# Kernel optimization log

Measured on AMD Instinct MI355X. Metric: run time of the kernel, lower is better.

The kernel has to match this reference:

```python
import jax, jax.numpy as jnp
import numpy as np

NUM_HEADS = 8
DEPTH_K = 256
DEPTH_V = 256


def rel_to_abs(x):
    # x: [B, Nh, L, 2L-1] -> [B, Nh, L, L] via the pad/reshape skew trick
    B, Nh, L, _ = x.shape
    x = jnp.pad(x, ((0, 0), (0, 0), (0, 0), (0, 1)))            # [B,Nh,L,2L]
    flat = x.reshape(B, Nh, L * 2 * L)
    flat = jnp.pad(flat, ((0, 0), (0, 0), (0, L - 1)))
    final = flat.reshape(B, Nh, L + 1, 2 * L - 1)
    return final[:, :, :L, L - 1:]


def relative_logits_1d(q, rel_k, H, W, transpose_mask):
    # q: [B, Nh, H, W, d]; rel_k: [2W-1, d]
    B, Nh = q.shape[0], q.shape[1]
    rel = jnp.einsum('bhxyd,md->bhxym', q, rel_k)               # [B,Nh,H,W,2W-1]
    rel = rel.reshape(B, Nh * H, W, 2 * W - 1)
    rel = rel_to_abs(rel)                                       # [B,Nh*H,W,W]
    rel = rel.reshape(B, Nh, H, W, W)
    rel = jnp.broadcast_to(rel[:, :, :, None, :, :], (B, Nh, H, H, W, W))
    rel = jnp.transpose(rel, transpose_mask)
    return rel.reshape(B, Nh, H * W, H * W)


def split_heads_2d(x):
    B, H, W, c = x.shape
    x = x.reshape(B, H, W, NUM_HEADS, c // NUM_HEADS)
    return jnp.transpose(x, (0, 3, 1, 2, 4))                     # [B,Nh,H,W,d]


def setup_inputs() -> dict:
    key = jax.random.key(0)
    k1, k2, k3 = jax.random.split(key, 3)
    dk_head = DEPTH_K // NUM_HEADS
    H = W = 32
    inputs = jax.random.normal(k1, (8, H, W, 2 * DEPTH_K + DEPTH_V), dtype=jnp.float32)
    key_rel_w = jax.random.normal(k2, (2 * W - 1, dk_head), dtype=jnp.float32) * dk_head ** -0.5
    key_rel_h = jax.random.normal(k3, (2 * H - 1, dk_head), dtype=jnp.float32) * dk_head ** -0.5
    return {"inputs": inputs, "key_rel_w": key_rel_w, "key_rel_h": key_rel_h}


def reference(inputs, key_rel_w, key_rel_h):
    B, H, W, _ = inputs.shape
    q, k, v = jnp.split(inputs, [DEPTH_K, 2 * DEPTH_K], axis=-1)
    q = split_heads_2d(q) * (DEPTH_K / NUM_HEADS) ** -0.5        # [B,Nh,H,W,dk]
    k = split_heads_2d(k)
    v = split_heads_2d(v)

    flat_q = q.reshape(B, NUM_HEADS, H * W, -1)
    flat_k = k.reshape(B, NUM_HEADS, H * W, -1)
    flat_v = v.reshape(B, NUM_HEADS, H * W, -1)

    logits = jnp.einsum('bnqd,bnkd->bnqk', flat_q, flat_k)       # [B,Nh,HW,HW]
    w_rel = relative_logits_1d(q, key_rel_w, H, W, (0, 1, 2, 4, 3, 5))
    h_rel = relative_logits_1d(jnp.transpose(q, (0, 1, 3, 2, 4)), key_rel_h,
                               W, H, (0, 1, 4, 2, 5, 3))
    logits = logits + h_rel + w_rel

    weights = jax.nn.softmax(logits, axis=-1)
    attn = jnp.einsum('bnqk,bnkd->bnqd', weights, flat_v)        # [B,Nh,HW,dv]
    attn = attn.reshape(B, NUM_HEADS, H, W, -1)
    out = jnp.transpose(attn, (0, 2, 3, 1, 4)).reshape(B, H, W, DEPTH_V)
    return out
```

## Files before the change

### kernel.cpp

```cpp
#include <hip/hip_runtime.h>
#include <hip/hip_bf16.h>

typedef short bf16x8 __attribute__((ext_vector_type(8)));
typedef float f32x4  __attribute__((ext_vector_type(4)));

#define DEVINL static __device__ __forceinline__

DEVINL unsigned short f2bf(float x){
  union { float f; unsigned u; } v; v.f = x;
  unsigned r = v.u + 0x7fffu + ((v.u >> 16) & 1u);
  return (unsigned short)(r >> 16);
}
DEVINL float bf2f(unsigned short b){
  union { unsigned u; float f; } v; v.u = ((unsigned)b) << 16; return v.f;
}
DEVINL unsigned pk2(float a, float b){
  __hip_bfloat162 h = __float22bfloat162_rn(float2{a, b});
  union { __hip_bfloat162 h2; unsigned u; } cv; cv.h2 = h; return cv.u;
}
DEVINL float fexp2(float x){
  float r; asm("v_exp_f32 %0, %1" : "=v"(r) : "v"(x)); return r;
}

__global__ __launch_bounds__(512, 4)
void aug_attn_kernel(const float* __restrict__ inp,
                     const float* __restrict__ relw,
                     const float* __restrict__ relh,
                     float* __restrict__ out)
{
  __shared__ __align__(16) unsigned short s_rw[128*66];
  __shared__ __align__(16) unsigned short s_rh[128*34];
  __shared__ __align__(16) unsigned short s_k [2][128*40];
  __shared__ __align__(16) unsigned short s_vt[2][4096];

  const int tid  = threadIdx.x;
  const int wv   = tid >> 6;
  const int lane = tid & 63;
  const int lo16 = lane & 15;
  const int hi4  = lane >> 4;

  const int bid = blockIdx.x;
  const int bn  = bid >> 3;
  const int qc  = bid & 7;
  const int b   = bn >> 3;
  const int n   = bn & 7;
  const int x1l = wv >> 1;
  const int qh  = wv & 1;
  const int x1  = qc*4 + x1l;
  const int y1  = qh*16 + lo16;
  const int qrow = x1l*32 + y1;

  const float qscale = 0.17677669529663687f;
  const float L2E    = 1.44269504088896f;
  const float MFIX   = 8.0f;

  const int krow = tid >> 2;
  const int c8   = (tid & 3) * 8;
  const float* kptr = inp + ((size_t)(b*1024 + krow))*768 + 256 + n*32 + c8;
  const float* vptr = kptr + 256;
  const size_t kstep = (size_t)128*768;

  float4 kA = *(const float4*)kptr;
  float4 kB = *(const float4*)(kptr+4);
  float4 vA = *(const float4*)vptr;
  float4 vB = *(const float4*)(vptr+4);

  const int vst = krow >> 6, vkr = krow & 63;
  int vslot[8];
#pragma unroll
  for (int j=0;j<8;++j){
    const int dv = c8 + j;
    vslot[j] = vst*2048 + dv*64 + (((vkr>>3) ^ (dv&7) ^ ((dv>>3)&3))<<3) + (vkr&7);
  }

  bf16x8 qf;
  {
    const float* qp = inp + ((size_t)((b*32 + x1)*32 + y1))*768 + n*32 + hi4*8;
    float4 a = *(const float4*)qp;
    float4 c = *(const float4*)(qp+4);
    union { unsigned u[4]; bf16x8 v; } cv;
    cv.u[0]=pk2(a.x*qscale, a.y*qscale);
    cv.u[1]=pk2(a.z*qscale, a.w*qscale);
    cv.u[2]=pk2(c.x*qscale, c.y*qscale);
    cv.u[3]=pk2(c.z*qscale, c.w*qscale);
    qf = cv.v;
  }

#pragma unroll
  for (int mt=0; mt<4; ++mt){
    const int m = mt*16 + lo16;
    bf16x8 rf = {0,0,0,0,0,0,0,0};
    if (m < 63){
      const float* rp = relw + m*32 + hi4*8;
      float4 a = *(const float4*)rp;
      float4 c = *(const float4*)(rp+4);
      union { unsigned u[4]; bf16x8 v; } cv;
      cv.u[0]=pk2(a.x,a.y); cv.u[1]=pk2(a.z,a.w);
      cv.u[2]=pk2(c.x,c.y); cv.u[3]=pk2(c.z,c.w);
      rf = cv.v;
    }
    f32x4 acc = {0.f,0.f,0.f,0.f};
    acc = __builtin_amdgcn_mfma_f32_16x16x32_bf16(qf, rf, acc, 0,0,0);
    const int rw0 = x1l*32 + qh*16 + hi4*4;
#pragma unroll
    for (int r=0;r<4;++r)
      s_rw[(rw0+r)*66 + m] = f2bf(acc[r]);
  }

#pragma unroll
  for (int mt=0; mt<4; ++mt){
    const int m = mt*16 + lo16;
    bf16x8 rf = {0,0,0,0,0,0,0,0};
    if (m < 63){
      const float* rp = relh + m*32 + hi4*8;
      float4 a = *(const float4*)rp;
      float4 c = *(const float4*)(rp+4);
      union { unsigned u[4]; bf16x8 v; } cv;
      cv.u[0]=pk2(a.x,a.y); cv.u[1]=pk2(a.z,a.w);
      cv.u[2]=pk2(c.x,c.y); cv.u[3]=pk2(c.z,c.w);
      rf = cv.v;
    }
    const int x2 = m + x1 - 31;
    f32x4 acc = {0.f,0.f,0.f,0.f};
    acc = __builtin_amdgcn_mfma_f32_16x16x32_bf16(qf, rf, acc, 0,0,0);
    if (x2 >= 0 && x2 < 32){
      const int rw0 = x1l*32 + qh*16 + hi4*4;
#pragma unroll
      for (int r=0;r<4;++r)
        s_rh[(rw0+r)*34 + x2] = f2bf(acc[r]);
    }
  }

  float rwl2[2][4];
  {
    const int mb = 31 - y1 + 4*hi4;
#pragma unroll
    for (int p=0;p<2;++p)
#pragma unroll
      for (int r=0;r<4;++r)
        rwl2[p][r] = (bf2f(s_rw[qrow*66 + mb + 16*p + r]) - MFIX)*L2E;
  }

  float l_run = 0.f;
  f32x4 accO[2];
  {
    f32x4 z = {0.f,0.f,0.f,0.f};
    accO[0] = z; accO[1] = z;
  }

  for (int ph=0; ph<8; ++ph){
    const int cur = ph & 1;
    {
      uint4 kw; kw.x=pk2(kA.x,kA.y); kw.y=pk2(kA.z,kA.w);
                kw.z=pk2(kB.x,kB.y); kw.w=pk2(kB.z,kB.w);
      *(uint4*)(&s_k[cur][krow*40 + c8]) = kw;
      const unsigned u0=pk2(vA.x,vA.y), u1=pk2(vA.z,vA.w);
      const unsigned u2=pk2(vB.x,vB.y), u3=pk2(vB.z,vB.w);
      unsigned short* vt = s_vt[cur];
      vt[vslot[0]]=(unsigned short)u0;  vt[vslot[1]]=(unsigned short)(u0>>16);
      vt[vslot[2]]=(unsigned short)u1;  vt[vslot[3]]=(unsigned short)(u1>>16);
      vt[vslot[4]]=(unsigned short)u2;  vt[vslot[5]]=(unsigned short)(u2>>16);
      vt[vslot[6]]=(unsigned short)u3;  vt[vslot[7]]=(unsigned short)(u3>>16);
    }
    asm volatile("s_waitcnt lgkmcnt(0)" ::: "memory");
    __builtin_amdgcn_s_barrier();
    asm volatile("" ::: "memory");

    if (ph < 7){
      kptr += kstep; vptr += kstep;
      kA = *(const float4*)kptr; kB = *(const float4*)(kptr+4);
      vA = *(const float4*)vptr; vB = *(const float4*)(vptr+4);
    }

#pragma unroll
    for (int st=0; st<2; ++st){
      bf16x8 kfrag[4];
#pragma unroll
      for (int kt=0;kt<4;++kt)
        kfrag[kt] = *(const bf16x8*)(&s_k[cur][(st*64 + kt*16 + lo16)*40 + hi4*8]);
      bf16x8 vfrag[2][2];
#pragma unroll
      for (int dvt=0;dvt<2;++dvt){
        const int dv = dvt*16 + lo16;
        const int xr = (dv&7) ^ ((dv>>3)&3);
#pragma unroll
        for (int kc=0;kc<2;++kc){
          const int blk = (kc*4 + hi4) ^ xr;
          vfrag[dvt][kc] = *(const bf16x8*)(&s_vt[cur][st*2048 + dv*64 + blk*8]);
        }
      }

      f32x4 S[4];
      __builtin_amdgcn_s_setprio(1);
#pragma unroll
      for (int kt=0;kt<4;++kt){
        f32x4 z = {0.f,0.f,0.f,0.f};
        S[kt] = __builtin_amdgcn_mfma_f32_16x16x32_bf16(kfrag[kt], qf, z, 0,0,0);
      }
      __builtin_amdgcn_s_setprio(0);

      const unsigned rhu = *(const unsigned*)(&s_rh[qrow*34 + 4*ph + 2*st]);
      const float rh0L = bf2f((unsigned short)(rhu & 0xffffu))*L2E;
      const float rh1L = bf2f((unsigned short)(rhu >> 16))*L2E;
      unsigned W[4][2];
      float lacc = 0.f;
#pragma unroll
      for (int kt=0;kt<4;++kt){
        const float rhL = (kt<2)? rh0L : rh1L;
        const int p = kt & 1;
        float pv0 = fexp2(__builtin_fmaf(S[kt][0], L2E, rwl2[p][0] + rhL));
        float pv1 = fexp2(__builtin_fmaf(S[kt][1], L2E, rwl2[p][1] + rhL));
        float pv2 = fexp2(__builtin_fmaf(S[kt][2], L2E, rwl2[p][2] + rhL));
        float pv3 = fexp2(__builtin_fmaf(S[kt][3], L2E, rwl2[p][3] + rhL));
        lacc += (pv0+pv1) + (pv2+pv3);
        W[kt][0] = pk2(pv0, pv1);
        W[kt][1] = pk2(pv2, pv3);
      }
      l_run += lacc;

      bf16x8 pfrag[2];
#pragma unroll
      for (int kc=0;kc<2;++kc){
        unsigned r0 = W[2*kc][0],   r1 = W[2*kc][1];
        unsigned r2 = W[2*kc+1][0], r3 = W[2*kc+1][1];
        asm("v_permlane32_swap_b32 %0, %1" : "+v"(r0), "+v"(r2));
        asm("v_permlane32_swap_b32 %0, %1" : "+v"(r1), "+v"(r3));
        asm("v_permlane16_swap_b32 %0, %1" : "+v"(r0), "+v"(r2));
        asm("v_permlane16_swap_b32 %0, %1" : "+v"(r1), "+v"(r3));
        union { unsigned u[4]; bf16x8 v; } cv;
        cv.u[0]=r0; cv.u[1]=r1; cv.u[2]=r2; cv.u[3]=r3;
        pfrag[kc] = cv.v;
      }

      __builtin_amdgcn_s_setprio(1);
#pragma unroll
      for (int kc=0;kc<2;++kc)
#pragma unroll
        for (int dvt=0;dvt<2;++dvt)
          accO[dvt] = __builtin_amdgcn_mfma_f32_16x16x32_bf16(
                        vfrag[dvt][kc], pfrag[kc], accO[dvt], 0,0,0);
      __builtin_amdgcn_s_setprio(0);
    }
  }

  float l = l_run;
  l += __shfl_xor(l, 16, 64);
  l += __shfl_xor(l, 32, 64);
  const float inv = 1.f / l;
  float* op = out + ((size_t)((b*32 + x1)*32 + y1))*256 + n*32;
#pragma unroll
  for (int dvt=0;dvt<2;++dvt){
    float4 o;
    o.x = accO[dvt][0]*inv;
    o.y = accO[dvt][1]*inv;
    o.z = accO[dvt][2]*inv;
    o.w = accO[dvt][3]*inv;
    *(float4*)(op + dvt*16 + hi4*4) = o;
  }
}

extern "C" void kernel_launch(void* const* d_in, const int* in_sizes, int n_in,
                              void* d_out, int out_size, void* d_ws, size_t ws_size,
                              hipStream_t stream) {
  (void)in_sizes; (void)n_in; (void)d_ws; (void)ws_size; (void)out_size;
  const float* inp  = (const float*)d_in[0];
  const float* relw = (const float*)d_in[1];
  const float* relh = (const float*)d_in[2];
  float* out = (float*)d_out;
  dim3 grid(512), block(512);
  aug_attn_kernel<<<grid, block, 0, stream>>>(inp, relw, relh, out);
}
```

Baseline: 100.7 us.

## Deepen K/V prefetch to two stages, remap blocks per XCD, drop setprio

Global loads for K/V now run two tiles ahead using two register sets, and the LDS store for the next tile moves to the end of each phase, after the compute. This hides more global-load latency behind the MFMA and exp work. The block index is remapped so that the eight query chunks of one (batch, head) land on the same XCD, which improves L2 reuse of K/V. The s_setprio hints are removed and the phase loop is fully unrolled, at the cost of higher register pressure that could reduce occupancy.

```diff
diff --git a/kernel.cpp b/kernel.cpp
--- a/kernel.cpp
+++ b/kernel.cpp
@@ -39,9 +39,11 @@
   const int lo16 = lane & 15;
   const int hi4  = lane >> 4;
 
-  const int bid = blockIdx.x;
-  const int bn  = bid >> 3;
-  const int qc  = bid & 7;
+  const int p   = blockIdx.x;
+  const int xcd = p & 7;
+  const int j   = p >> 3;
+  const int bn  = xcd*8 + (j >> 3);
+  const int qc  = j & 7;
   const int b   = bn >> 3;
   const int n   = bn & 7;
   const int x1l = wv >> 1;
@@ -56,22 +58,24 @@
 
   const int krow = tid >> 2;
   const int c8   = (tid & 3) * 8;
-  const float* kptr = inp + ((size_t)(b*1024 + krow))*768 + 256 + n*32 + c8;
-  const float* vptr = kptr + 256;
+  const float* kbase = inp + ((size_t)(b*1024 + krow))*768 + 256 + n*32 + c8;
   const size_t kstep = (size_t)128*768;
-
-  float4 kA = *(const float4*)kptr;
-  float4 kB = *(const float4*)(kptr+4);
-  float4 vA = *(const float4*)vptr;
-  float4 vB = *(const float4*)(vptr+4);
 
   const int vst = krow >> 6, vkr = krow & 63;
   int vslot[8];
 #pragma unroll
-  for (int j=0;j<8;++j){
-    const int dv = c8 + j;
-    vslot[j] = vst*2048 + dv*64 + (((vkr>>3) ^ (dv&7) ^ ((dv>>3)&3))<<3) + (vkr&7);
-  }
+  for (int jj=0;jj<8;++jj){
+    const int dv = c8 + jj;
+    vslot[jj] = vst*2048 + dv*64 + (((vkr>>3) ^ (dv&7) ^ ((dv>>3)&3))<<3) + (vkr&7);
+  }
+
+  float4 kR0a, kR0b, vR0a, vR0b;
+  float4 kR1a, kR1b, vR1a, vR1b;
+
+  kR0a = *(const float4*)(kbase);
+  kR0b = *(const float4*)(kbase+4);
+  vR0a = *(const float4*)(kbase+256);
+  vR0b = *(const float4*)(kbase+260);
 
   bf16x8 qf;
   {
@@ -135,10 +139,30 @@
   {
     const int mb = 31 - y1 + 4*hi4;
 #pragma unroll
-    for (int p=0;p<2;++p)
+    for (int pp=0;pp<2;++pp)
 #pragma unroll
       for (int r=0;r<4;++r)
-        rwl2[p][r] = (bf2f(s_rw[qrow*66 + mb + 16*p + r]) - MFIX)*L2E;
+        rwl2[pp][r] = (bf2f(s_rw[qrow*66 + mb + 16*pp + r]) - MFIX)*L2E;
+  }
+
+  {
+    uint4 kw; kw.x=pk2(kR0a.x,kR0a.y); kw.y=pk2(kR0a.z,kR0a.w);
+              kw.z=pk2(kR0b.x,kR0b.y); kw.w=pk2(kR0b.z,kR0b.w);
+    *(uint4*)(&s_k[0][krow*40 + c8]) = kw;
+    const unsigned u0=pk2(vR0a.x,vR0a.y), u1=pk2(vR0a.z,vR0a.w);
+    const unsigned u2=pk2(vR0b.x,vR0b.y), u3=pk2(vR0b.z,vR0b.w);
+    unsigned short* vt = s_vt[0];
+    vt[vslot[0]]=(unsigned short)u0;  vt[vslot[1]]=(unsigned short)(u0>>16);
+    vt[vslot[2]]=(unsigned short)u1;  vt[vslot[3]]=(unsigned short)(u1>>16);
+    vt[vslot[4]]=(unsigned short)u2;  vt[vslot[5]]=(unsigned short)(u2>>16);
+    vt[vslot[6]]=(unsigned short)u3;  vt[vslot[7]]=(unsigned short)(u3>>16);
+  }
+  {
+    const float* kp = kbase + kstep;
+    kR1a = *(const float4*)(kp);
+    kR1b = *(const float4*)(kp+4);
+    vR1a = *(const float4*)(kp+256);
+    vR1b = *(const float4*)(kp+260);
   }
 
   float l_run = 0.f;
@@ -148,28 +172,22 @@
     accO[0] = z; accO[1] = z;
   }
 
+#pragma unroll
   for (int ph=0; ph<8; ++ph){
     const int cur = ph & 1;
-    {
-      uint4 kw; kw.x=pk2(kA.x,kA.y); kw.y=pk2(kA.z,kA.w);
-                kw.z=pk2(kB.x,kB.y); kw.w=pk2(kB.z,kB.w);
-      *(uint4*)(&s_k[cur][krow*40 + c8]) = kw;
-      const unsigned u0=pk2(vA.x,vA.y), u1=pk2(vA.z,vA.w);
-      const unsigned u2=pk2(vB.x,vB.y), u3=pk2(vB.z,vB.w);
-      unsigned short* vt = s_vt[cur];
-      vt[vslot[0]]=(unsigned short)u0;  vt[vslot[1]]=(unsigned short)(u0>>16);
-      vt[vslot[2]]=(unsigned short)u1;  vt[vslot[3]]=(unsigned short)(u1>>16);
-      vt[vslot[4]]=(unsigned short)u2;  vt[vslot[5]]=(unsigned short)(u2>>16);
-      vt[vslot[6]]=(unsigned short)u3;  vt[vslot[7]]=(unsigned short)(u3>>16);
-    }
     asm volatile("s_waitcnt lgkmcnt(0)" ::: "memory");
     __builtin_amdgcn_s_barrier();
     asm volatile("" ::: "memory");
 
-    if (ph < 7){
-      kptr += kstep; vptr += kstep;
-      kA = *(const float4*)kptr; kB = *(const float4*)(kptr+4);
-      vA = *(const float4*)vptr; vB = *(const float4*)(vptr+4);
+    if (ph < 6){
+      const float* kp = kbase + (size_t)(ph+2)*kstep;
+      if (cur == 0){
+        kR0a = *(const float4*)(kp);   kR0b = *(const float4*)(kp+4);
+        vR0a = *(const float4*)(kp+256); vR0b = *(const float4*)(kp+260);
+      } else {
+        kR1a = *(const float4*)(kp);   kR1b = *(const float4*)(kp+4);
+        vR1a = *(const float4*)(kp+256); vR1b = *(const float4*)(kp+260);
+      }
     }
 
 #pragma unroll
@@ -191,13 +209,11 @@
       }
 
       f32x4 S[4];
-      __builtin_amdgcn_s_setprio(1);
 #pragma unroll
       for (int kt=0;kt<4;++kt){
         f32x4 z = {0.f,0.f,0.f,0.f};
         S[kt] = __builtin_amdgcn_mfma_f32_16x16x32_bf16(kfrag[kt], qf, z, 0,0,0);
       }
-      __builtin_amdgcn_s_setprio(0);
 
       const unsigned rhu = *(const unsigned*)(&s_rh[qrow*34 + 4*ph + 2*st]);
       const float rh0L = bf2f((unsigned short)(rhu & 0xffffu))*L2E;
@@ -207,11 +223,11 @@
 #pragma unroll
       for (int kt=0;kt<4;++kt){
         const float rhL = (kt<2)? rh0L : rh1L;
-        const int p = kt & 1;
-        float pv0 = fexp2(__builtin_fmaf(S[kt][0], L2E, rwl2[p][0] + rhL));
-        float pv1 = fexp2(__builtin_fmaf(S[kt][1], L2E, rwl2[p][1] + rhL));
-        float pv2 = fexp2(__builtin_fmaf(S[kt][2], L2E, rwl2[p][2] + rhL));
-        float pv3 = fexp2(__builtin_fmaf(S[kt][3], L2E, rwl2[p][3] + rhL));
+        const int pp = kt & 1;
+        float pv0 = fexp2(__builtin_fmaf(S[kt][0], L2E, rwl2[pp][0] + rhL));
+        float pv1 = fexp2(__builtin_fmaf(S[kt][1], L2E, rwl2[pp][1] + rhL));
+        float pv2 = fexp2(__builtin_fmaf(S[kt][2], L2E, rwl2[pp][2] + rhL));
+        float pv3 = fexp2(__builtin_fmaf(S[kt][3], L2E, rwl2[pp][3] + rhL));
         lacc += (pv0+pv1) + (pv2+pv3);
         W[kt][0] = pk2(pv0, pv1);
         W[kt][1] = pk2(pv2, pv3);
@@ -232,14 +248,29 @@
         pfrag[kc] = cv.v;
       }
 
-      __builtin_amdgcn_s_setprio(1);
 #pragma unroll
       for (int kc=0;kc<2;++kc)
 #pragma unroll
         for (int dvt=0;dvt<2;++dvt)
           accO[dvt] = __builtin_amdgcn_mfma_f32_16x16x32_bf16(
                         vfrag[dvt][kc], pfrag[kc], accO[dvt], 0,0,0);
-      __builtin_amdgcn_s_setprio(0);
+    }
+
+    if (ph < 7){
+      const int nxt = cur ^ 1;
+      float4 ka, kb2, va, vb2;
+      if (nxt == 0){ ka=kR0a; kb2=kR0b; va=vR0a; vb2=vR0b; }
+      else         { ka=kR1a; kb2=kR1b; va=vR1a; vb2=vR1b; }
+      uint4 kw; kw.x=pk2(ka.x,ka.y); kw.y=pk2(ka.z,ka.w);
+                kw.z=pk2(kb2.x,kb2.y); kw.w=pk2(kb2.z,kb2.w);
+      *(uint4*)(&s_k[nxt][krow*40 + c8]) = kw;
+      const unsigned u0=pk2(va.x,va.y), u1=pk2(va.z,va.w);
+      const unsigned u2=pk2(vb2.x,vb2.y), u3=pk2(vb2.z,vb2.w);
+      unsigned short* vt = s_vt[nxt];
+      vt[vslot[0]]=(unsigned short)u0;  vt[vslot[1]]=(unsigned short)(u0>>16);
+      vt[vslot[2]]=(unsigned short)u1;  vt[vslot[3]]=(unsigned short)(u1>>16);
+      vt[vslot[4]]=(unsigned short)u2;  vt[vslot[5]]=(unsigned short)(u2>>16);
+      vt[vslot[6]]=(unsigned short)u3;  vt[vslot[7]]=(unsigned short)(u3>>16);
     }
   }
 
```

New measurement: 178.0 us. +76.7%, slower.
